# Kernel tuning notes

Hardware: AMD Instinct MI355X
Metric: run time of the kernel (lower is better)

## Reference

```python
import jax, jax.numpy as jnp
import numpy as np

B, M, C, D, FF, FEAT = 1, 1024, 128, 512, 1024, 20
PAIR = 3 * D + 2 * FEAT  # slow_scorer_size = 1576


def _ffnn(x, W0, b0, W1, b1):
    # FFNN(depth=1): hidden relu layer then linear output (eval mode, no dropout)
    return jax.nn.relu(x @ W0 + b0) @ W1 + b1


def _batch_gather(x, idx):
    # x: [B, M, ...], idx: [B, ...] int -> gather along mention dim per batch
    return jax.vmap(lambda xb, ib: xb[ib])(x, idx)


def _bucket_distance(d):
    # log-scale distance buckets 0..9 (identity for d<=4)
    log_idx = jnp.floor(jnp.log(jnp.maximum(d, 1).astype(jnp.float32)) / jnp.log(2.0)).astype(jnp.int32) + 3
    return jnp.clip(jnp.where(d <= 4, d, log_idx), 0, 9)


def setup_inputs() -> dict:
    key = jax.random.key(0)
    ks = jax.random.split(key, 10)
    s = 0.02
    return {
        'mention_emb': jax.random.normal(ks[0], (B, M, D), dtype=jnp.float32),
        'mention_cluster_ids': jax.random.randint(ks[1], (B, M), 0, 200),
        'mention_speaker_ids': jax.random.randint(ks[2], (B, M), 0, 2),
        'ms_W0': jax.random.normal(ks[3], (D, FF), dtype=jnp.float32) * s,
        'ms_b0': jnp.zeros((FF,), jnp.float32),
        'ms_W1': jax.random.normal(ks[4], (FF, 1), dtype=jnp.float32) * s,
        'ms_b1': jnp.zeros((1,), jnp.float32),
        'sp_W0': jax.random.normal(ks[5], (PAIR, FF), dtype=jnp.float32) * s,
        'sp_b0': jnp.zeros((FF,), jnp.float32),
        'sp_W1': jax.random.normal(ks[6], (FF, 1), dtype=jnp.float32) * s,
        'sp_b1': jnp.zeros((1,), jnp.float32),
        'speaker_emb': jax.random.normal(ks[7], (2, FEAT), dtype=jnp.float32) * s,
        'bucket_emb': jax.random.normal(ks[8], (10, FEAT), dtype=jnp.float32) * s,
    }


def reference(mention_emb, mention_cluster_ids, mention_speaker_ids,
              ms_W0, ms_b0, ms_W1, ms_b1,
              sp_W0, sp_b0, sp_W1, sp_b1,
              speaker_emb, bucket_emb):
    # mention scoring
    mention_scores = _ffnn(mention_emb, ms_W0, ms_b0, ms_W1, ms_b1)[..., 0]  # [B, M]

    # get_antecedent_info: fixed window of C previous mentions
    offsets = jnp.arange(1, C + 1)[None, None, :]                    # [1,1,C]
    raw = jnp.arange(M)[None, :, None] - offsets                      # [1,M,C]
    antecedents = jnp.broadcast_to(jnp.clip(raw, 0, M - 1), (B, M, C))
    ant_mask = jnp.broadcast_to(raw >= 0, (B, M, C))

    fast_scores = _batch_gather(mention_scores, antecedents) + mention_scores[:, :, None]
    antecedent_emb = _batch_gather(mention_emb, antecedents)          # [B,M,C,D]

    # slow pair scorer features
    same_speaker = (_batch_gather(mention_speaker_ids, antecedents) == mention_speaker_ids[:, :, None]).astype(jnp.int32)
    speaker_feat = speaker_emb[same_speaker]                          # [B,M,C,FEAT]
    bucket_feat = jnp.broadcast_to(bucket_emb[_bucket_distance(offsets)], (B, M, C, FEAT))

    src = jnp.broadcast_to(mention_emb[:, :, None, :], (B, M, C, D))
    pair_emb = jnp.concatenate([src, antecedent_emb, src * antecedent_emb, speaker_feat, bucket_feat], axis=-1)
    slow_scores = _ffnn(pair_emb, sp_W0, sp_b0, sp_W1, sp_b1)[..., 0]  # [B,M,C]

    antecedent_scores = fast_scores + slow_scores + jnp.log(ant_mask.astype(jnp.float32))
    overall_scores = jnp.concatenate([jnp.zeros((B, M, 1), jnp.float32), antecedent_scores], axis=2)
    overall_dist = jax.nn.softmax(overall_scores, axis=-1)
    eps = 1e-6
    overall_dist = jnp.clip(overall_dist, eps, 1.0 - eps)
    overall_dist = overall_dist / jnp.sum(overall_dist, axis=-1, keepdims=True)

    # coref loss from cluster ids
    ant_cluster = _batch_gather(mention_cluster_ids, antecedents) * ant_mask.astype(mention_cluster_ids.dtype)
    same_cluster = ant_cluster == mention_cluster_ids[:, :, None]
    non_dummy = (mention_cluster_ids > 0)[:, :, None]
    ant_labels = same_cluster & non_dummy
    dummy_labels = ~jnp.any(ant_labels, axis=2, keepdims=True)
    overall_labels = jnp.concatenate([dummy_labels, ant_labels], axis=2)
    loss = -jnp.sum(jnp.log(overall_dist) * overall_labels.astype(jnp.float32), axis=2)
    loss = jnp.mean(jnp.sum(loss, axis=1))
    return overall_dist, loss
```

## Files before the change

### kernel.cpp

```cpp
#include <hip/hip_runtime.h>
#include <math.h>

#define MM 1024
#define DD 512
#define CC 128
#define LDSR 516


typedef __attribute__((ext_vector_type(8))) short bf16x8;
typedef __attribute__((ext_vector_type(4), aligned(8))) short bf16x4a;
typedef __attribute__((ext_vector_type(4))) float f32x4;
typedef __attribute__((ext_vector_type(16))) float f32x16;

__device__ __forceinline__ ushort bf16_rn(float x) {
    uint u = __float_as_uint(x);
    uint r = u + 0x7fffu + ((u >> 16) & 1u);
    return (ushort)(r >> 16);
}
__device__ __forceinline__ float bf16_to_f(ushort u) {
    return __uint_as_float(((uint)u) << 16);
}
__device__ __forceinline__ bf16x8 ld_lds16(const ushort* p) {
    bf16x4a lo = *(const bf16x4a*)p;
    bf16x4a hi = *(const bf16x4a*)(p + 4);
    return __builtin_shufflevector(lo, hi, 0, 1, 2, 3, 4, 5, 6, 7);
}

__global__ __launch_bounds__(256) void prep_emb(const float* __restrict__ emb,
                                                ushort* __restrict__ embb)
{
    int i = blockIdx.x * 256 + threadIdx.x;
    float2 v = ((const float2*)emb)[i];
    ushort2 o;
    o.x = bf16_rn(v.x);
    o.y = bf16_rn(v.y);
    ((ushort2*)embb)[i] = o;
}

__global__ __launch_bounds__(256) void prep_wall(const float* __restrict__ ms_W0,
                                                 const float* __restrict__ sp_W0,
                                                 ushort* __restrict__ Wall)
{
    __shared__ float t[64][65];
    const int k0 = blockIdx.x * 64;
    const int n0 = blockIdx.y * 64;
    const int g = n0 >> 10;
    const float* src = (g == 0) ? ms_W0 : (sp_W0 + (size_t)(g - 1) * 512 * 1024);
    const int col0 = n0 & 1023;
    const int tr = threadIdx.x >> 6, tc = threadIdx.x & 63;
#pragma unroll
    for (int i = 0; i < 16; ++i) {
        int k = tr + i * 4;
        t[k][tc] = src[(size_t)(k0 + k) * 1024 + col0 + tc];
    }
    __syncthreads();
    const int f = threadIdx.x >> 2;
    const int c4 = threadIdx.x & 3;
    ushort tmp[16];
#pragma unroll
    for (int j = 0; j < 16; ++j) tmp[j] = bf16_rn(t[c4 * 16 + j][f]);
    uint4* dst = (uint4*)(Wall + (size_t)(n0 + f) * 512 + k0 + c4 * 16);
    dst[0] = *(uint4*)&tmp[0];
    dst[1] = *(uint4*)&tmp[8];
}

__global__ __launch_bounds__(64) void prep_wfrag(const float* __restrict__ sp_W0,
                                                 ushort* __restrict__ Wfrag)
{
    const int ts = blockIdx.x;
    const int l = threadIdx.x;
    const int tt = ts >> 5, s = ts & 31;
    const int f = tt * 32 + (l & 31);
    const int kb = s * 16 + (l >> 5) * 8;
    const float* W = sp_W0 + (size_t)1024 * 1024;
    ushort tmp[8];
#pragma unroll
    for (int j = 0; j < 8; ++j) tmp[j] = bf16_rn(W[(size_t)(kb + j) * 1024 + f]);
    uint4* dst = (uint4*)(Wfrag + ((size_t)ts * 64 + l) * 8);
    *dst = *(uint4*)&tmp[0];
}

__global__ __launch_bounds__(256) void gemm_h_mfma(
    const ushort* __restrict__ embb, const ushort* __restrict__ Wall,
    float* __restrict__ H)
{
    const int n0 = blockIdx.x * 128;
    const int m0 = blockIdx.y * 128;
    const int lane = threadIdx.x & 63, wave = threadIdx.x >> 6;
    const int wx = wave & 1, wy = wave >> 1;
    const int l15 = lane & 15, lq = lane >> 4;

    const ushort* arow[4];
#pragma unroll
    for (int mi = 0; mi < 4; ++mi)
        arow[mi] = embb + (size_t)(m0 + wy * 64 + mi * 16 + l15) * 512;
    const ushort* brow[4];
#pragma unroll
    for (int ni = 0; ni < 4; ++ni)
        brow[ni] = Wall + (size_t)(n0 + wx * 64 + ni * 16 + l15) * 512;

    f32x4 acc[4][4];
#pragma unroll
    for (int i = 0; i < 4; ++i)
#pragma unroll
        for (int j = 0; j < 4; ++j) acc[i][j] = (f32x4)0.f;

    for (int kt = 0; kt < 512; kt += 32) {
        const int ko = kt + lq * 8;
        bf16x8 av[4], bv[4];
#pragma unroll
        for (int mi = 0; mi < 4; ++mi) av[mi] = *(const bf16x8*)(arow[mi] + ko);
#pragma unroll
        for (int ni = 0; ni < 4; ++ni) bv[ni] = *(const bf16x8*)(brow[ni] + ko);
#pragma unroll
        for (int mi = 0; mi < 4; ++mi)
#pragma unroll
            for (int ni = 0; ni < 4; ++ni)
                acc[mi][ni] = __builtin_amdgcn_mfma_f32_16x16x32_bf16(av[mi], bv[ni], acc[mi][ni], 0, 0, 0);
    }
#pragma unroll
    for (int mi = 0; mi < 4; ++mi)
#pragma unroll
        for (int r = 0; r < 4; ++r) {
            int mrow = m0 + wy * 64 + mi * 16 + lq * 4 + r;
#pragma unroll
            for (int ni = 0; ni < 4; ++ni)
                H[(size_t)mrow * 3072 + n0 + wx * 64 + ni * 16 + l15] = acc[mi][ni][r];
        }
}

__global__ void small_proj(const float* __restrict__ speaker_emb,
                           const float* __restrict__ bucket_emb,
                           const float* __restrict__ sp_W0,
                           float* __restrict__ spk_proj, float* __restrict__ bkt_proj)
{
    int r = blockIdx.x;
    const float* e; const float* W; float* out;
    if (r < 2) { e = speaker_emb + r * 20; W = sp_W0 + (size_t)1536 * 1024; out = spk_proj + r * 1024; }
    else       { e = bucket_emb + (r - 2) * 20; W = sp_W0 + (size_t)1556 * 1024; out = bkt_proj + (r - 2) * 1024; }
    float ek[20];
#pragma unroll
    for (int k = 0; k < 20; ++k) ek[k] = e[k];
    for (int f = threadIdx.x; f < 1024; f += blockDim.x) {
        float s = 0.f;
#pragma unroll
        for (int k = 0; k < 20; ++k) s = fmaf(ek[k], W[(size_t)k * 1024 + f], s);
        out[f] = s;
    }
}

__global__ __launch_bounds__(256) void mention_score(
    const float* __restrict__ H, const float* __restrict__ ms_b0,
    const float* __restrict__ ms_W1, const float* __restrict__ ms_b1,
    float* __restrict__ ms)
{
    int m = blockIdx.x;
    float v = 0.f;
    for (int f = threadIdx.x; f < 1024; f += 256) {
        float h = H[(size_t)m * 3072 + f] + ms_b0[f];
        v += fmaxf(h, 0.f) * ms_W1[f];
    }
#pragma unroll
    for (int o = 1; o < 64; o <<= 1) v += __shfl_xor(v, o);
    __shared__ float sm[4];
    if ((threadIdx.x & 63) == 0) sm[threadIdx.x >> 6] = v;
    __syncthreads();
    if (threadIdx.x == 0) ms[m] = sm[0] + sm[1] + sm[2] + sm[3] + ms_b1[0];
}

__global__ __launch_bounds__(1024, 4) void pair_mfma(
    const ushort* __restrict__ embb, const ushort* __restrict__ Wfrag,
    const float* __restrict__ H, const float* __restrict__ spk_proj,
    const float* __restrict__ bkt_proj, const float* __restrict__ sp_b0,
    const float* __restrict__ sp_W1, const int* __restrict__ speaker,
    float* __restrict__ slow)
{
    extern __shared__ ushort Alds[];
    float* red = (float*)(Alds + 128 * LDSR);
    int* meta_ss = (int*)(red + 16 * 128);
    int* meta_bk = meta_ss + 128;
    const int m = blockIdx.x;
    const int tid = threadIdx.x;
    const int spk_m = speaker[m];

    {
        const int c = tid >> 3;
        const int kh = (tid & 7) * 64;
        int a = m - 1 - c; if (a < 0) a = 0;
        const ushort* ea = embb + (size_t)a * 512 + kh;
        const ushort* em = embb + (size_t)m * 512 + kh;
        ushort* dst = Alds + c * LDSR + kh;
#pragma unroll
        for (int j = 0; j < 64; j += 8) {
            bf16x8 va = *(const bf16x8*)(ea + j);
            bf16x8 vm = *(const bf16x8*)(em + j);
            uint pr[4];
#pragma unroll
            for (int p = 0; p < 4; ++p) {
                float q0 = bf16_to_f((ushort)va[2 * p])     * bf16_to_f((ushort)vm[2 * p]);
                float q1 = bf16_to_f((ushort)va[2 * p + 1]) * bf16_to_f((ushort)vm[2 * p + 1]);
                pr[p] = __builtin_amdgcn_perm(__float_as_uint(q1), __float_as_uint(q0), 0x07060302u);
            }
            *(uint2*)(dst + j)     = *(uint2*)&pr[0];
            *(uint2*)(dst + j + 4) = *(uint2*)&pr[2];
        }
        if ((tid & 7) == 0) {
            meta_ss[c] = (speaker[a] == spk_m) ? 1 : 0;
            int off = c + 1;
            int bk;
            if (off <= 4) bk = off;
            else { bk = 31 - __clz(off) + 3; if (bk > 9) bk = 9; }
            meta_bk[c] = bk;
        }
    }
    __syncthreads();

    const int lane = tid & 63;
    const int wave = __builtin_amdgcn_readfirstlane(tid >> 6);
    const int l31 = lane & 31, k5 = lane >> 5;
    const int f0 = wave * 64;

    const ushort* bb = Wfrag + (size_t)(wave * 2) * 16384 + (size_t)lane * 8;
    const ushort* ab = Alds + l31 * LDSR + k5 * 8;

    for (int pass = 0; pass < 2; ++pass) {
        const int c0 = pass * 64;
        const ushort* ap = ab + c0 * LDSR;
        f32x16 acc[2][2];
#pragma unroll
        for (int i = 0; i < 2; ++i)
#pragma unroll
            for (int j = 0; j < 2; ++j) acc[i][j] = (f32x16)0.f;

#pragma unroll 2
        for (int s = 0; s < 32; ++s) {
            bf16x8 b0 = *(const bf16x8*)(bb + s * 512);
            bf16x8 b1 = *(const bf16x8*)(bb + 16384 + s * 512);
            bf16x8 a0 = ld_lds16(ap + s * 16);
            bf16x8 a1 = ld_lds16(ap + 32 * LDSR + s * 16);
            acc[0][0] = __builtin_amdgcn_mfma_f32_32x32x16_bf16(a0, b0, acc[0][0], 0, 0, 0);
            acc[0][1] = __builtin_amdgcn_mfma_f32_32x32x16_bf16(a0, b1, acc[0][1], 0, 0, 0);
            acc[1][0] = __builtin_amdgcn_mfma_f32_32x32x16_bf16(a1, b0, acc[1][0], 0, 0, 0);
            acc[1][1] = __builtin_amdgcn_mfma_f32_32x32x16_bf16(a1, b1, acc[1][1], 0, 0, 0);
        }

        float srcb[2], w1v[2], sp0v[2], sp1v[2], bk9v[2];
#pragma unroll
        for (int ni = 0; ni < 2; ++ni) {
            int fcol = f0 + ni * 32 + l31;
            srcb[ni] = H[(size_t)m * 3072 + 1024 + fcol] + sp_b0[fcol];
            w1v[ni]  = sp_W1[fcol];
            sp0v[ni] = spk_proj[fcol];
            sp1v[ni] = spk_proj[1024 + fcol];
            bk9v[ni] = bkt_proj[9 * 1024 + fcol];
        }
#pragma unroll
        for (int mi = 0; mi < 2; ++mi) {
#pragma unroll
            for (int reg = 0; reg < 16; ++reg) {
                const int c = c0 + mi * 32 + 4 * k5 + (reg & 3) + 8 * (reg >> 2);
                int a = m - 1 - c; if (a < 0) a = 0;
                const int ss = meta_ss[c];
                const float* antp = H + (size_t)a * 3072 + 2048;
                float s = 0.f;
#pragma unroll
                for (int ni = 0; ni < 2; ++ni) {
                    const int fcol = f0 + ni * 32 + l31;
                    float bval = pass ? bk9v[ni] : bkt_proj[(size_t)meta_bk[c] * 1024 + fcol];
                    float pre = acc[mi][ni][reg] + srcb[ni] + antp[fcol] + (ss ? sp1v[ni] : sp0v[ni]) + bval;
                    s += fmaxf(pre, 0.f) * w1v[ni];
                }
                s += __shfl_xor(s, 1); s += __shfl_xor(s, 2); s += __shfl_xor(s, 4);
                s += __shfl_xor(s, 8); s += __shfl_xor(s, 16);
                if (l31 == 0) red[wave * 128 + c] = s;
            }
        }
    }
    __syncthreads();
    if (tid < 128) {
        float s = 0.f;
#pragma unroll
        for (int i = 0; i < 16; ++i) s += red[i * 128 + tid];
        slow[(size_t)m * 128 + tid] = s;
    }
}

__device__ __forceinline__ float bsum2(float v, float* sm) {
#pragma unroll
    for (int o = 1; o < 64; o <<= 1) v += __shfl_xor(v, o);
    __syncthreads();
    if ((threadIdx.x & 63) == 0) sm[threadIdx.x >> 6] = v;
    __syncthreads();
    return sm[0] + sm[1];
}
__device__ __forceinline__ float bmax2(float v, float* sm) {
#pragma unroll
    for (int o = 1; o < 64; o <<= 1) v = fmaxf(v, __shfl_xor(v, o));
    __syncthreads();
    if ((threadIdx.x & 63) == 0) sm[threadIdx.x >> 6] = v;
    __syncthreads();
    return fmaxf(sm[0], sm[1]);
}

__global__ __launch_bounds__(128) void softmax_loss(
    const float* __restrict__ slow, const float* __restrict__ ms,
    const float* __restrict__ sp_b1, const int* __restrict__ cluster,
    float* __restrict__ out, float* __restrict__ loss_partial)
{
    const int m = blockIdx.x, c = threadIdx.x;
    __shared__ float sm[2];
    const int raw = m - 1 - c;
    const bool maskv = raw >= 0;
    const int a = maskv ? raw : 0;
    float score = slow[(size_t)m * 128 + c] + sp_b1[0] + ms[m] + ms[a];
    if (!maskv) score = -INFINITY;

    float mx = fmaxf(bmax2(score, sm), 0.f);
    float e = expf(score - mx);
    float e0 = expf(0.f - mx);
    float sum = bsum2(e, sm) + e0;
    float p = e / sum, p0 = e0 / sum;
    const float eps = 1e-6f;
    p  = fminf(fmaxf(p,  eps), 1.f - eps);
    p0 = fminf(fmaxf(p0, eps), 1.f - eps);
    float sum2 = bsum2(p, sm) + p0;
    p /= sum2; p0 /= sum2;
    out[(size_t)m * 129 + 1 + c] = p;
    if (c == 0) out[(size_t)m * 129] = p0;

    const int cid = cluster[m];
    const bool lbl = maskv && (cid > 0) && (cluster[a] == cid);
    float anyc = bsum2(lbl ? 1.f : 0.f, sm);
    float lsum = bsum2(lbl ? -logf(p) : 0.f, sm);
    if (c == 0) {
        if (anyc == 0.f) lsum += -logf(p0);
        loss_partial[m] = lsum;
    }
}

__global__ void loss_sum(const float* __restrict__ lp, float* __restrict__ out) {
    float v = 0.f;
    for (int i = threadIdx.x; i < 1024; i += 256) v += lp[i];
#pragma unroll
    for (int o = 1; o < 64; o <<= 1) v += __shfl_xor(v, o);
    __shared__ float sm[4];
    if ((threadIdx.x & 63) == 0) sm[threadIdx.x >> 6] = v;
    __syncthreads();
    if (threadIdx.x == 0) out[(size_t)1024 * 129] = sm[0] + sm[1] + sm[2] + sm[3];
}

extern "C" void kernel_launch(void* const* d_in, const int* in_sizes, int n_in,
                              void* d_out, int out_size, void* d_ws, size_t ws_size,
                              hipStream_t stream)
{
    const float* emb   = (const float*)d_in[0];
    const int*   clus  = (const int*)  d_in[1];
    const int*   spk   = (const int*)  d_in[2];
    const float* ms_W0 = (const float*)d_in[3];
    const float* ms_b0 = (const float*)d_in[4];
    const float* ms_W1 = (const float*)d_in[5];
    const float* ms_b1 = (const float*)d_in[6];
    const float* sp_W0 = (const float*)d_in[7];
    const float* sp_b0 = (const float*)d_in[8];
    const float* sp_W1 = (const float*)d_in[9];
    const float* sp_b1 = (const float*)d_in[10];
    const float* spke  = (const float*)d_in[11];
    const float* bkte  = (const float*)d_in[12];

    float* ws = (float*)d_ws;
    float* H        = ws;
    float* slow     = ws + 3145728;
    float* spk_proj = ws + 3276800;
    float* bkt_proj = ws + 3278848;
    float* msc      = ws + 3289088;
    float* lossp    = ws + 3290112;
    ushort* embb    = (ushort*)(ws + 3291136);
    ushort* Wall    = (ushort*)(ws + 3553280);
    ushort* Wfrag   = Wall + (size_t)3072 * 512;
    float* out = (float*)d_out;

    const int pair_lds = 128 * LDSR * 2 + 16 * 128 * 4 + 256 * 4;

    static bool attr_set = false;
    if (!attr_set) {
        hipFuncSetAttribute((const void*)pair_mfma,
                            hipFuncAttributeMaxDynamicSharedMemorySize,
                            pair_lds);
        attr_set = true;
    }

    hipLaunchKernelGGL(prep_emb, dim3(1024), dim3(256), 0, stream, emb, embb);
    hipLaunchKernelGGL(prep_wall, dim3(8, 48), dim3(256), 0, stream, ms_W0, sp_W0, Wall);
    hipLaunchKernelGGL(prep_wfrag, dim3(1024), dim3(64), 0, stream, sp_W0, Wfrag);
    hipLaunchKernelGGL(gemm_h_mfma, dim3(24, 8), dim3(256), 0, stream, embb, Wall, H);
    hipLaunchKernelGGL(small_proj, dim3(12), dim3(256), 0, stream, spke, bkte, sp_W0, spk_proj, bkt_proj);
    hipLaunchKernelGGL(mention_score, dim3(1024), dim3(256), 0, stream, H, ms_b0, ms_W1, ms_b1, msc);
    hipLaunchKernelGGL(pair_mfma, dim3(1024), dim3(1024), pair_lds, stream,
                       embb, Wfrag, H, spk_proj, bkt_proj, sp_b0, sp_W1, spk, slow);
    hipLaunchKernelGGL(softmax_loss, dim3(1024), dim3(128), 0, stream,
                       slow, msc, sp_b1, clus, out, lossp);
    hipLaunchKernelGGL(loss_sum, dim3(1), dim3(256), 0, stream, lossp, out);
}
```

Measured before the change: 374.4 us.

## Store antecedent projection in bf16, double-buffer pair GEMM loads, stagger k-order per wave

The GEMM epilogue now splits H into an fp32 buffer for the mention and source projections and a separate bf16 buffer for the antecedent projection. This halves the gather traffic in the pair kernel's epilogue, at some cost in precision for that term. The pair kernel's MFMA loop becomes explicitly double-buffered, prefetching the next step's A and B fragments, and starts each group of waves at a different k offset so they do not all hit the same weight rows at once. The prologue thread mapping is also changed so adjacent threads handle different antecedents.

After: 390.7 us. +4.3%, slower.

```diff
diff --git a/kernel.cpp b/kernel.cpp
--- a/kernel.cpp
+++ b/kernel.cpp
@@ -82,7 +82,7 @@
 
 __global__ __launch_bounds__(256) void gemm_h_mfma(
     const ushort* __restrict__ embb, const ushort* __restrict__ Wall,
-    float* __restrict__ H)
+    float* __restrict__ H2, ushort* __restrict__ antb)
 {
     const int n0 = blockIdx.x * 128;
     const int m0 = blockIdx.y * 128;
@@ -118,15 +118,28 @@
             for (int ni = 0; ni < 4; ++ni)
                 acc[mi][ni] = __builtin_amdgcn_mfma_f32_16x16x32_bf16(av[mi], bv[ni], acc[mi][ni], 0, 0, 0);
     }
-#pragma unroll
-    for (int mi = 0; mi < 4; ++mi)
-#pragma unroll
-        for (int r = 0; r < 4; ++r) {
-            int mrow = m0 + wy * 64 + mi * 16 + lq * 4 + r;
-#pragma unroll
-            for (int ni = 0; ni < 4; ++ni)
-                H[(size_t)mrow * 3072 + n0 + wx * 64 + ni * 16 + l15] = acc[mi][ni][r];
-        }
+    if (n0 < 2048) {
+#pragma unroll
+        for (int mi = 0; mi < 4; ++mi)
+#pragma unroll
+            for (int r = 0; r < 4; ++r) {
+                int mrow = m0 + wy * 64 + mi * 16 + lq * 4 + r;
+#pragma unroll
+                for (int ni = 0; ni < 4; ++ni)
+                    H2[(size_t)mrow * 2048 + n0 + wx * 64 + ni * 16 + l15] = acc[mi][ni][r];
+            }
+    } else {
+#pragma unroll
+        for (int mi = 0; mi < 4; ++mi)
+#pragma unroll
+            for (int r = 0; r < 4; ++r) {
+                int mrow = m0 + wy * 64 + mi * 16 + lq * 4 + r;
+#pragma unroll
+                for (int ni = 0; ni < 4; ++ni)
+                    antb[(size_t)mrow * 1024 + (n0 - 2048) + wx * 64 + ni * 16 + l15] =
+                        bf16_rn(acc[mi][ni][r]);
+            }
+    }
 }
 
 __global__ void small_proj(const float* __restrict__ speaker_emb,
@@ -150,14 +163,14 @@
 }
 
 __global__ __launch_bounds__(256) void mention_score(
-    const float* __restrict__ H, const float* __restrict__ ms_b0,
+    const float* __restrict__ H2, const float* __restrict__ ms_b0,
     const float* __restrict__ ms_W1, const float* __restrict__ ms_b1,
     float* __restrict__ ms)
 {
     int m = blockIdx.x;
     float v = 0.f;
     for (int f = threadIdx.x; f < 1024; f += 256) {
-        float h = H[(size_t)m * 3072 + f] + ms_b0[f];
+        float h = H2[(size_t)m * 2048 + f] + ms_b0[f];
         v += fmaxf(h, 0.f) * ms_W1[f];
     }
 #pragma unroll
@@ -170,10 +183,10 @@
 
 __global__ __launch_bounds__(1024, 4) void pair_mfma(
     const ushort* __restrict__ embb, const ushort* __restrict__ Wfrag,
-    const float* __restrict__ H, const float* __restrict__ spk_proj,
-    const float* __restrict__ bkt_proj, const float* __restrict__ sp_b0,
-    const float* __restrict__ sp_W1, const int* __restrict__ speaker,
-    float* __restrict__ slow)
+    const float* __restrict__ H2, const ushort* __restrict__ antb,
+    const float* __restrict__ spk_proj, const float* __restrict__ bkt_proj,
+    const float* __restrict__ sp_b0, const float* __restrict__ sp_W1,
+    const int* __restrict__ speaker, float* __restrict__ slow)
 {
     extern __shared__ ushort Alds[];
     float* red = (float*)(Alds + 128 * LDSR);
@@ -184,8 +197,8 @@
     const int spk_m = speaker[m];
 
     {
-        const int c = tid >> 3;
-        const int kh = (tid & 7) * 64;
+        const int c = tid & 127;
+        const int kh = (tid >> 7) * 64;
         int a = m - 1 - c; if (a < 0) a = 0;
         const ushort* ea = embb + (size_t)a * 512 + kh;
         const ushort* em = embb + (size_t)m * 512 + kh;
@@ -204,13 +217,15 @@
             *(uint2*)(dst + j)     = *(uint2*)&pr[0];
             *(uint2*)(dst + j + 4) = *(uint2*)&pr[2];
         }
-        if ((tid & 7) == 0) {
-            meta_ss[c] = (speaker[a] == spk_m) ? 1 : 0;
-            int off = c + 1;
+        if (tid < 128) {
+            const int cc = tid;
+            int aa = m - 1 - cc; if (aa < 0) aa = 0;
+            meta_ss[cc] = (speaker[aa] == spk_m) ? 1 : 0;
+            int off = cc + 1;
             int bk;
             if (off <= 4) bk = off;
             else { bk = 31 - __clz(off) + 3; if (bk > 9) bk = 9; }
-            meta_bk[c] = bk;
+            meta_bk[cc] = bk;
         }
     }
     __syncthreads();
@@ -219,6 +234,7 @@
     const int wave = __builtin_amdgcn_readfirstlane(tid >> 6);
     const int l31 = lane & 31, k5 = lane >> 5;
     const int f0 = wave * 64;
+    const int srot = (wave >> 2) * 8;
 
     const ushort* bb = Wfrag + (size_t)(wave * 2) * 16384 + (size_t)lane * 8;
     const ushort* ab = Alds + l31 * LDSR + k5 * 8;
@@ -232,23 +248,34 @@
 #pragma unroll
             for (int j = 0; j < 2; ++j) acc[i][j] = (f32x16)0.f;
 
+        bf16x8 av[2][2], bv[2][2];
+#pragma unroll
+        for (int p = 0; p < 2; ++p) {
+            const int ss = (p + srot) & 31;
+            bv[p][0] = *(const bf16x8*)(bb + ss * 512);
+            bv[p][1] = *(const bf16x8*)(bb + 16384 + ss * 512);
+            av[p][0] = ld_lds16(ap + ss * 16);
+            av[p][1] = ld_lds16(ap + 32 * LDSR + ss * 16);
+        }
 #pragma unroll 2
-        for (int s = 0; s < 32; ++s) {
-            bf16x8 b0 = *(const bf16x8*)(bb + s * 512);
-            bf16x8 b1 = *(const bf16x8*)(bb + 16384 + s * 512);
-            bf16x8 a0 = ld_lds16(ap + s * 16);
-            bf16x8 a1 = ld_lds16(ap + 32 * LDSR + s * 16);
-            acc[0][0] = __builtin_amdgcn_mfma_f32_32x32x16_bf16(a0, b0, acc[0][0], 0, 0, 0);
-            acc[0][1] = __builtin_amdgcn_mfma_f32_32x32x16_bf16(a0, b1, acc[0][1], 0, 0, 0);
-            acc[1][0] = __builtin_amdgcn_mfma_f32_32x32x16_bf16(a1, b0, acc[1][0], 0, 0, 0);
-            acc[1][1] = __builtin_amdgcn_mfma_f32_32x32x16_bf16(a1, b1, acc[1][1], 0, 0, 0);
+        for (int i = 0; i < 32; ++i) {
+            const int cur = i & 1;
+            acc[0][0] = __builtin_amdgcn_mfma_f32_32x32x16_bf16(av[cur][0], bv[cur][0], acc[0][0], 0, 0, 0);
+            acc[0][1] = __builtin_amdgcn_mfma_f32_32x32x16_bf16(av[cur][0], bv[cur][1], acc[0][1], 0, 0, 0);
+            acc[1][0] = __builtin_amdgcn_mfma_f32_32x32x16_bf16(av[cur][1], bv[cur][0], acc[1][0], 0, 0, 0);
+            acc[1][1] = __builtin_amdgcn_mfma_f32_32x32x16_bf16(av[cur][1], bv[cur][1], acc[1][1], 0, 0, 0);
+            const int ss = (i + 2 + srot) & 31;
+            bv[cur][0] = *(const bf16x8*)(bb + ss * 512);
+            bv[cur][1] = *(const bf16x8*)(bb + 16384 + ss * 512);
+            av[cur][0] = ld_lds16(ap + ss * 16);
+            av[cur][1] = ld_lds16(ap + 32 * LDSR + ss * 16);
         }
 
         float srcb[2], w1v[2], sp0v[2], sp1v[2], bk9v[2];
 #pragma unroll
         for (int ni = 0; ni < 2; ++ni) {
             int fcol = f0 + ni * 32 + l31;
-            srcb[ni] = H[(size_t)m * 3072 + 1024 + fcol] + sp_b0[fcol];
+            srcb[ni] = H2[(size_t)m * 2048 + 1024 + fcol] + sp_b0[fcol];
             w1v[ni]  = sp_W1[fcol];
             sp0v[ni] = spk_proj[fcol];
             sp1v[ni] = spk_proj[1024 + fcol];
@@ -260,14 +287,15 @@
             for (int reg = 0; reg < 16; ++reg) {
                 const int c = c0 + mi * 32 + 4 * k5 + (reg & 3) + 8 * (reg >> 2);
                 int a = m - 1 - c; if (a < 0) a = 0;
-                const int ss = meta_ss[c];
-                const float* antp = H + (size_t)a * 3072 + 2048;
+                const int ss2 = meta_ss[c];
+                const ushort* antp = antb + (size_t)a * 1024;
                 float s = 0.f;
 #pragma unroll
                 for (int ni = 0; ni < 2; ++ni) {
                     const int fcol = f0 + ni * 32 + l31;
                     float bval = pass ? bk9v[ni] : bkt_proj[(size_t)meta_bk[c] * 1024 + fcol];
-                    float pre = acc[mi][ni][reg] + srcb[ni] + antp[fcol] + (ss ? sp1v[ni] : sp0v[ni]) + bval;
+                    float antv = bf16_to_f(antp[fcol]);
+                    float pre = acc[mi][ni][reg] + srcb[ni] + antv + (ss2 ? sp1v[ni] : sp0v[ni]) + bval;
                     s += fmaxf(pre, 0.f) * w1v[ni];
                 }
                 s += __shfl_xor(s, 1); s += __shfl_xor(s, 2); s += __shfl_xor(s, 4);
@@ -368,15 +396,16 @@
     const float* bkte  = (const float*)d_in[12];
 
     float* ws = (float*)d_ws;
-    float* H        = ws;
-    float* slow     = ws + 3145728;
-    float* spk_proj = ws + 3276800;
-    float* bkt_proj = ws + 3278848;
-    float* msc      = ws + 3289088;
-    float* lossp    = ws + 3290112;
-    ushort* embb    = (ushort*)(ws + 3291136);
-    ushort* Wall    = (ushort*)(ws + 3553280);
-    ushort* Wfrag   = Wall + (size_t)3072 * 512;
+    float*  H2       = ws;
+    ushort* antb     = (ushort*)(ws + 2097152);
+    float*  slow     = ws + 2621440;
+    float*  spk_proj = ws + 2752512;
+    float*  bkt_proj = ws + 2754560;
+    float*  msc      = ws + 2764800;
+    float*  lossp    = ws + 2765824;
+    ushort* embb     = (ushort*)(ws + 2766848);
+    ushort* Wall     = (ushort*)(ws + 3028992);
+    ushort* Wfrag    = Wall + (size_t)3072 * 512;
     float* out = (float*)d_out;
 
     const int pair_lds = 128 * LDSR * 2 + 16 * 128 * 4 + 256 * 4;
@@ -392,11 +421,11 @@
     hipLaunchKernelGGL(prep_emb, dim3(1024), dim3(256), 0, stream, emb, embb);
     hipLaunchKernelGGL(prep_wall, dim3(8, 48), dim3(256), 0, stream, ms_W0, sp_W0, Wall);
     hipLaunchKernelGGL(prep_wfrag, dim3(1024), dim3(64), 0, stream, sp_W0, Wfrag);
-    hipLaunchKernelGGL(gemm_h_mfma, dim3(24, 8), dim3(256), 0, stream, embb, Wall, H);
+    hipLaunchKernelGGL(gemm_h_mfma, dim3(24, 8), dim3(256), 0, stream, embb, Wall, H2, antb);
     hipLaunchKernelGGL(small_proj, dim3(12), dim3(256), 0, stream, spke, bkte, sp_W0, spk_proj, bkt_proj);
-    hipLaunchKernelGGL(mention_score, dim3(1024), dim3(256), 0, stream, H, ms_b0, ms_W1, ms_b1, msc);
+    hipLaunchKernelGGL(mention_score, dim3(1024), dim3(256), 0, stream, H2, ms_b0, ms_W1, ms_b1, msc);
     hipLaunchKernelGGL(pair_mfma, dim3(1024), dim3(1024), pair_lds, stream,
-                       embb, Wfrag, H, spk_proj, bkt_proj, sp_b0, sp_W1, spk, slow);
+                       embb, Wfrag, H2, antb, spk_proj, bkt_proj, sp_b0, sp_W1, spk, slow);
     hipLaunchKernelGGL(softmax_loss, dim3(1024), dim3(128), 0, stream,
                        slow, msc, sp_b1, clus, out, lossp);
     hipLaunchKernelGGL(loss_sum, dim3(1), dim3(256), 0, stream, lossp, out);
```
